# Optimization experiments

Measured on AMD Instinct MI355X. Metric: run time of the kernel, lower is better.

## Reference

```python
import jax, jax.numpy as jnp
import numpy as np

N_TH1 = 30
LB = 1e-20
UB = 1e20
LB_EXP = -20.0
UB_EXP = 20.0


def make_directions(n_th1):
    # Reproduces the TF __init__ direction sampling on the sphere.
    n_th2 = 2 * (n_th1 - 1) + 1
    th1 = np.linspace(-np.pi / 2, np.pi / 2, n_th1)
    th2 = np.linspace(-np.pi, np.pi, n_th2)
    c1, s1 = np.cos(th1), np.sin(th1)
    c2, s2 = np.cos(th2), np.sin(th2)
    dx = np.outer(c1[1:-1], c2[:-1])          # [n_th1-2, n_th2-1]
    dy = np.outer(c1[1:-1], s2[:-1])
    dz = np.broadcast_to(s1[1:-1, None], dx.shape)
    mid = np.stack([dx, dy, dz], -1).reshape(-1, 3)
    poles = np.array([[c1[0] * c2[0], c1[0] * s2[0], s1[0]],
                      [c1[-1] * c2[0], c1[-1] * s2[0], s1[-1]]])
    return np.concatenate([mid, poles], 0).astype(np.float32)  # [D, 3]


def setup_inputs() -> dict:
    key = jax.random.key(0)
    k1, k2, k3 = jax.random.split(key, 3)
    vertices = jax.random.normal(k1, (8, 64, 32, 3), jnp.float32)
    # smoothness is a p-norm exponent; realistic range [2, 20]
    smoothness = 2.0 + 18.0 * jax.random.uniform(k2, (8, 64), jnp.float32)
    pointcloud = jax.random.normal(k3, (8, 2048, 3), jnp.float32)
    return {"vertices": vertices, "smoothness": smoothness, "pointcloud": pointcloud}


def _spt_forward(vertices, smoothness):
    dirs = jnp.asarray(make_directions(N_TH1))            # [D, 3]
    B, P = vertices.shape[0], vertices.shape[1]
    mean_v = jnp.mean(vertices, axis=2, keepdims=True)    # [B,P,1,3]
    local_v = vertices - mean_v                           # [B,P,V,3]

    # z = <v, x> for every vertex/direction pair -> [B,P,V,D]
    z = jnp.einsum('bpvc,dc->bpvd', local_v, dirs)
    zm = jnp.maximum(z, 0.0)
    p = smoothness[:, :, None, None]                      # [B,P,1,1]

    # dynamic rescaling k = 10^ceil(...) to keep zm^p in fp range
    zm_max = jnp.max(zm, axis=2, keepdims=True)           # [B,P,1,D]
    zm_log = jnp.log(zm_max) / jnp.log(10.0)              # = max over V of log10(zm)
    exponent = zm_log * p
    lk = jnp.where(exponent < LB_EXP, (-15.0 - exponent) / p, 0.0)
    k = 10.0 ** jnp.clip(jnp.ceil(lk), 0.0, UB_EXP)       # [B,P,1,D]
    k = jax.lax.stop_gradient(k)                          # ceil has zero grad anyway

    zm = zm * k
    pos = zm > 0
    # clip(zm^p, lb, ub) - (zm==0)*lb  ==  where(zm>0, clip(zm^p,lb,ub), 0)
    zm_p = jnp.where(pos, jnp.clip(jnp.where(pos, zm, 1.0) ** p, LB, UB), 0.0)
    sum_zm_p = jnp.sum(zm_p, axis=2, keepdims=True)       # [B,P,1,D]
    spos = sum_zm_p > 0
    h = jnp.where(spos, jnp.clip(jnp.where(spos, sum_zm_p, 1.0) ** (1.0 / p), LB, UB), LB)

    # dh/dz = clip((zm/h)^(p-1), lb, ub)
    ratio = zm / h                                        # [B,P,V,D]
    rpos = ratio > 0
    dhdz = jnp.where(rpos, jnp.clip(jnp.where(rpos, ratio, 1.0) ** (p - 1.0), LB, UB), LB)
    # dh/dx = dhdz^T @ vertices -> surface points
    dhdx = jnp.einsum('bpvd,bpvc->bpdc', dhdz, local_v)   # [B,P,D,3]
    surf = dhdx + mean_v                                  # broadcast [B,P,1,3]

    h_out = jnp.clip(h / k, -UB, UB)                      # [B,P,1,D]
    h_out = jnp.transpose(h_out, (0, 1, 3, 2))            # [B,P,D,1]
    local_dirs = jnp.broadcast_to(dirs[None, None], (B, P) + dirs.shape)
    direction_h = jnp.concatenate([local_dirs, h_out], axis=-1)  # [B,P,D,4]
    points = surf.reshape(B, -1, 3)                       # [B, P*D, 3]
    mean_out = mean_v.reshape(B, P, 3)
    return points, direction_h, mean_out, local_v


def reference(vertices, smoothness, pointcloud):
    points, direction_h, mean_out, local_v = _spt_forward(vertices, smoothness)
    B, P = vertices.shape[0], vertices.shape[1]
    # overlap / retraction loops are truncated in the source; placeholders
    overlap = jnp.zeros((B, P, 1), jnp.float32)
    retraction = jnp.zeros((B, P, 1), jnp.float32)
    return (points, direction_h, overlap, retraction, mean_out, local_v)
```

## Files before the change

### kernel.cpp

```cpp
#include <hip/hip_runtime.h>
#include <math.h>

#define NBP 512
#define VV 32
#define DD 1626
#define DHALF 813

#define O_POINTS 0
#define O_DIRH   2497536
#define O_OVER   5827584
#define O_RETR   5828096
#define O_MEAN   5828608
#define O_LOCAL  5830144

#define L10_2 0.3010299956639812f
#define L2_10 3.321928094887362f
#define LH_MIN -66.43856189774725f

__device__ __forceinline__ float fexp2(float x) {
  return __builtin_amdgcn_exp2f(x);
}

__device__ __forceinline__ void make_dir_fast(int d, float& x, float& y, float& z) {
  if (d < 1624) {
    const int i1 = d / 58 + 1;
    const int i2 = d - (i1 - 1) * 58;
    const float STEP = 0.10833078115826873f;
    const float th1 = -1.5707963267948966f + (float)i1 * STEP;
    const float th2 = -3.14159265358979323846f + (float)i2 * STEP;
    const float s1 = __sinf(th1);
    const float c1 = __cosf(th1);
    const float s2 = __sinf(th2);
    const float c2 = __cosf(th2);
    x = c1 * c2; y = c1 * s2; z = s1;
  } else if (d == 1624) {
    x = -6.123234e-17f; y = -7.49880e-33f; z = -1.0f;
  } else {
    x = -6.123234e-17f; y = -7.49880e-33f; z = 1.0f;
  }
}

__global__ __launch_bounds__(256) void spt_kernel(
    const float* __restrict__ vertices,
    const float* __restrict__ smooth,
    float* __restrict__ out)
{
  const int bp   = blockIdx.x;
  const int half = blockIdx.y;
  const int tid  = threadIdx.x;

  __shared__ __align__(16) float slvx[VV];
  __shared__ __align__(16) float slvy[VV];
  __shared__ __align__(16) float slvz[VV];

  const int dbase = half * DHALF;

  const int v = tid & 31;
  const float* vp = vertices + bp * (VV * 3) + v * 3;
  const float vx = vp[0], vy = vp[1], vz = vp[2];
  float sx = vx, sy = vy, sz = vz;
#pragma unroll
  for (int m = 16; m >= 1; m >>= 1) {
    sx += __shfl_xor(sx, m);
    sy += __shfl_xor(sy, m);
    sz += __shfl_xor(sz, m);
  }
  const float mx = sx * (1.0f / 32.0f);
  const float my = sy * (1.0f / 32.0f);
  const float mz = sz * (1.0f / 32.0f);
  if (tid < VV) {
    slvx[tid] = vx - mx;
    slvy[tid] = vy - my;
    slvz[tid] = vz - mz;
  }
  __syncthreads();

  if (half == 1) {
    if (tid < VV * 3) {
      const int vv = tid / 3, c = tid - vv * 3;
      const float val = (c == 0) ? slvx[vv] : ((c == 1) ? slvy[vv] : slvz[vv]);
      out[O_LOCAL + bp * (VV * 3) + tid] = val;
    }
    if (tid == 96) {
      out[O_MEAN + bp * 3 + 0] = mx;
      out[O_MEAN + bp * 3 + 1] = my;
      out[O_MEAN + bp * 3 + 2] = mz;
      out[O_OVER + bp] = 0.f;
      out[O_RETR + bp] = 0.f;
    }
  }

  const float p     = smooth[bp];
  const float inv_p = 1.0f / p;
  const float pm1   = p - 1.0f;
  const float plt   = p * L10_2;

  const float4* lvx4 = (const float4*)slvx;
  const float4* lvy4 = (const float4*)slvy;
  const float4* lvz4 = (const float4*)slvz;

  auto process = [&](int idx) {
    const int d = dbase + idx;
    float dx, dy, dz;
    make_dir_fast(d, dx, dy, dz);

    float w[VV];
    float zmax = 0.f;
#pragma unroll
    for (int j = 0; j < VV / 4; j++) {
      float4 X = lvx4[j], Y = lvy4[j], Z = lvz4[j];
      float z0 = fmaxf(fmaf(X.x, dx, fmaf(Y.x, dy, Z.x * dz)), 0.f);
      float z1 = fmaxf(fmaf(X.y, dx, fmaf(Y.y, dy, Z.y * dz)), 0.f);
      float z2 = fmaxf(fmaf(X.z, dx, fmaf(Y.z, dy, Z.z * dz)), 0.f);
      float z3 = fmaxf(fmaf(X.w, dx, fmaf(Y.w, dy, Z.w * dz)), 0.f);
      w[j * 4 + 0] = z0; w[j * 4 + 1] = z1;
      w[j * 4 + 2] = z2; w[j * 4 + 3] = z3;
      zmax = fmaxf(zmax, fmaxf(fmaxf(z0, z1), fmaxf(z2, z3)));
    }

    const float expo = __log2f(zmax) * plt;
    float kc = 0.f;
    if (expo < -20.f) {
      kc = fminf(fmaxf(ceilf((-15.f - expo) * inv_p), 0.f), 20.f);
    }
    const float kcl = kc * L2_10;
    const float A   = p * kcl;

    float s0 = 0.f, s1 = 0.f, s2 = 0.f, s3 = 0.f;
#pragma unroll
    for (int j = 0; j < VV / 4; j++) {
      float z0 = w[j * 4 + 0], z1 = w[j * 4 + 1];
      float z2 = w[j * 4 + 2], z3 = w[j * 4 + 3];
      float w0 = fexp2(fmaf(pm1, __log2f(z0), A));
      float w1 = fexp2(fmaf(pm1, __log2f(z1), A));
      float w2 = fexp2(fmaf(pm1, __log2f(z2), A));
      float w3 = fexp2(fmaf(pm1, __log2f(z3), A));
      s0 += w0 * z0;  s1 += w1 * z1;
      s2 += w2 * z2;  s3 += w3 * z3;
      w[j * 4 + 0] = w0; w[j * 4 + 1] = w1;
      w[j * 4 + 2] = w2; w[j * 4 + 3] = w3;
    }
    const float ssum = (s0 + s1) + (s2 + s3);

    float lh = LH_MIN;
    float C2 = 0.f;
    if (ssum > 0.f) {
      lh = inv_p * __log2f(ssum);
      C2 = fexp2(-fmaf(pm1, lh, kcl));
    }

    float ax = 0.f, ay = 0.f, az = 0.f;
#pragma unroll
    for (int j = 0; j < VV / 4; j++) {
      float4 X = lvx4[j], Y = lvy4[j], Z = lvz4[j];
      float w0 = w[j * 4 + 0], w1 = w[j * 4 + 1];
      float w2 = w[j * 4 + 2], w3 = w[j * 4 + 3];
      ax = fmaf(w0, X.x, fmaf(w1, X.y, fmaf(w2, X.z, fmaf(w3, X.w, ax))));
      ay = fmaf(w0, Y.x, fmaf(w1, Y.y, fmaf(w2, Y.z, fmaf(w3, Y.w, ay))));
      az = fmaf(w0, Z.x, fmaf(w1, Z.y, fmaf(w2, Z.z, fmaf(w3, Z.w, az))));
    }

    const int pbase = bp * DD + d;
    out[O_POINTS + pbase * 3 + 0] = fmaf(C2, ax, mx);
    out[O_POINTS + pbase * 3 + 1] = fmaf(C2, ay, my);
    out[O_POINTS + pbase * 3 + 2] = fmaf(C2, az, mz);

    float4 dvh = make_float4(dx, dy, dz, fexp2(lh - kcl));
    ((float4*)(out + O_DIRH))[pbase] = dvh;
  };

  process(tid);
  process(256 + tid);
  process(512 + tid);
  if (tid < DHALF - 768) process(768 + tid);
}

extern "C" void kernel_launch(void* const* d_in, const int* in_sizes, int n_in,
                              void* d_out, int out_size, void* d_ws, size_t ws_size,
                              hipStream_t stream) {
  const float* vertices = (const float*)d_in[0];
  const float* smooth   = (const float*)d_in[1];
  float* out = (float*)d_out;

  spt_kernel<<<dim3(NBP, 2), 256, 0, stream>>>(vertices, smooth, out);
}
```

Before: 76.37 us.

## Fuse weight and accumulation passes and split directions across four blocks

Drops the 32-entry per-thread weight array by recomputing the projections in a single fused loop. That loop computes the power weights, the normalizer sum and the weighted vertex sums together. This cuts register pressure so more waves can be resident, at the cost of recomputing the dot products. The grid also goes from 2 to 4 blocks per batch-point, each covering about 407 directions, which adds parallelism. The catch is that the second pass in each block leaves part of the threads idle.

```diff
diff --git a/kernel.cpp b/kernel.cpp
--- a/kernel.cpp
+++ b/kernel.cpp
@@ -4,7 +4,7 @@
 #define NBP 512
 #define VV 32
 #define DD 1626
-#define DHALF 813
+#define DSPAN 407
 
 #define O_POINTS 0
 #define O_DIRH   2497536
@@ -45,15 +45,16 @@
     const float* __restrict__ smooth,
     float* __restrict__ out)
 {
-  const int bp   = blockIdx.x;
-  const int half = blockIdx.y;
-  const int tid  = threadIdx.x;
+  const int bp  = blockIdx.x;
+  const int bz  = blockIdx.y;
+  const int tid = threadIdx.x;
 
   __shared__ __align__(16) float slvx[VV];
   __shared__ __align__(16) float slvy[VV];
   __shared__ __align__(16) float slvz[VV];
 
-  const int dbase = half * DHALF;
+  const int dbase = bz * DSPAN;
+  const int dend  = (DD - dbase) < DSPAN ? (DD - dbase) : DSPAN;
 
   const int v = tid & 31;
   const float* vp = vertices + bp * (VV * 3) + v * 3;
@@ -75,7 +76,7 @@
   }
   __syncthreads();
 
-  if (half == 1) {
+  if (bz == 1) {
     if (tid < VV * 3) {
       const int vv = tid / 3, c = tid - vv * 3;
       const float val = (c == 0) ? slvx[vv] : ((c == 1) ? slvy[vv] : slvz[vv]);
@@ -104,7 +105,6 @@
     float dx, dy, dz;
     make_dir_fast(d, dx, dy, dz);
 
-    float w[VV];
     float zmax = 0.f;
 #pragma unroll
     for (int j = 0; j < VV / 4; j++) {
@@ -113,8 +113,6 @@
       float z1 = fmaxf(fmaf(X.y, dx, fmaf(Y.y, dy, Z.y * dz)), 0.f);
       float z2 = fmaxf(fmaf(X.z, dx, fmaf(Y.z, dy, Z.z * dz)), 0.f);
       float z3 = fmaxf(fmaf(X.w, dx, fmaf(Y.w, dy, Z.w * dz)), 0.f);
-      w[j * 4 + 0] = z0; w[j * 4 + 1] = z1;
-      w[j * 4 + 2] = z2; w[j * 4 + 3] = z3;
       zmax = fmaxf(zmax, fmaxf(fmaxf(z0, z1), fmaxf(z2, z3)));
     }
 
@@ -126,38 +124,32 @@
     const float kcl = kc * L2_10;
     const float A   = p * kcl;
 
-    float s0 = 0.f, s1 = 0.f, s2 = 0.f, s3 = 0.f;
+    float ss0 = 0.f, ss1 = 0.f;
+    float ax = 0.f, ay = 0.f, az = 0.f;
 #pragma unroll
     for (int j = 0; j < VV / 4; j++) {
-      float z0 = w[j * 4 + 0], z1 = w[j * 4 + 1];
-      float z2 = w[j * 4 + 2], z3 = w[j * 4 + 3];
-      float w0 = fexp2(fmaf(pm1, __log2f(z0), A));
-      float w1 = fexp2(fmaf(pm1, __log2f(z1), A));
-      float w2 = fexp2(fmaf(pm1, __log2f(z2), A));
-      float w3 = fexp2(fmaf(pm1, __log2f(z3), A));
-      s0 += w0 * z0;  s1 += w1 * z1;
-      s2 += w2 * z2;  s3 += w3 * z3;
-      w[j * 4 + 0] = w0; w[j * 4 + 1] = w1;
-      w[j * 4 + 2] = w2; w[j * 4 + 3] = w3;
+      float4 X = lvx4[j], Y = lvy4[j], Z = lvz4[j];
+      float z0 = fmaxf(fmaf(X.x, dx, fmaf(Y.x, dy, Z.x * dz)), 0.f);
+      float z1 = fmaxf(fmaf(X.y, dx, fmaf(Y.y, dy, Z.y * dz)), 0.f);
+      float z2 = fmaxf(fmaf(X.z, dx, fmaf(Y.z, dy, Z.z * dz)), 0.f);
+      float z3 = fmaxf(fmaf(X.w, dx, fmaf(Y.w, dy, Z.w * dz)), 0.f);
+      float u0 = fexp2(fmaf(pm1, __log2f(z0), A));
+      float u1 = fexp2(fmaf(pm1, __log2f(z1), A));
+      float u2 = fexp2(fmaf(pm1, __log2f(z2), A));
+      float u3 = fexp2(fmaf(pm1, __log2f(z3), A));
+      ss0 = fmaf(u0, z0, ss0);  ss1 = fmaf(u1, z1, ss1);
+      ss0 = fmaf(u2, z2, ss0);  ss1 = fmaf(u3, z3, ss1);
+      ax = fmaf(u0, X.x, fmaf(u1, X.y, fmaf(u2, X.z, fmaf(u3, X.w, ax))));
+      ay = fmaf(u0, Y.x, fmaf(u1, Y.y, fmaf(u2, Y.z, fmaf(u3, Y.w, ay))));
+      az = fmaf(u0, Z.x, fmaf(u1, Z.y, fmaf(u2, Z.z, fmaf(u3, Z.w, az))));
     }
-    const float ssum = (s0 + s1) + (s2 + s3);
+    const float ssum = ss0 + ss1;
 
     float lh = LH_MIN;
     float C2 = 0.f;
     if (ssum > 0.f) {
       lh = inv_p * __log2f(ssum);
       C2 = fexp2(-fmaf(pm1, lh, kcl));
-    }
-
-    float ax = 0.f, ay = 0.f, az = 0.f;
-#pragma unroll
-    for (int j = 0; j < VV / 4; j++) {
-      float4 X = lvx4[j], Y = lvy4[j], Z = lvz4[j];
-      float w0 = w[j * 4 + 0], w1 = w[j * 4 + 1];
-      float w2 = w[j * 4 + 2], w3 = w[j * 4 + 3];
-      ax = fmaf(w0, X.x, fmaf(w1, X.y, fmaf(w2, X.z, fmaf(w3, X.w, ax))));
-      ay = fmaf(w0, Y.x, fmaf(w1, Y.y, fmaf(w2, Y.z, fmaf(w3, Y.w, ay))));
-      az = fmaf(w0, Z.x, fmaf(w1, Z.y, fmaf(w2, Z.z, fmaf(w3, Z.w, az))));
     }
 
     const int pbase = bp * DD + d;
@@ -170,9 +162,7 @@
   };
 
   process(tid);
-  process(256 + tid);
-  process(512 + tid);
-  if (tid < DHALF - 768) process(768 + tid);
+  if (tid + 256 < dend) process(256 + tid);
 }
 
 extern "C" void kernel_launch(void* const* d_in, const int* in_sizes, int n_in,
@@ -182,5 +172,5 @@
   const float* smooth   = (const float*)d_in[1];
   float* out = (float*)d_out;
 
-  spt_kernel<<<dim3(NBP, 2), 256, 0, stream>>>(vertices, smooth, out);
+  spt_kernel<<<dim3(NBP, 4), 256, 0, stream>>>(vertices, smooth, out);
 }
```

Result: no change. 77.70 us (+1.7%).
